# Performance work log

Hardware: AMD Instinct MI355X
Metric: run time of the kernel (lower is better)

## Reference

```python
import jax, jax.numpy as jnp
import numpy as np

B, S, D, M = 8, 32, 256, 2048
TOPK = 8

def setup_inputs() -> dict:
    key = jax.random.key(0)
    ks = jax.random.split(key, 10)
    def lin(kw, fan_in, fan_out):
        # kaiming normal (linear): std = 1/sqrt(fan_in); stored as [in, out]
        return jax.random.normal(kw, (fan_in, fan_out), jnp.float32) / jnp.sqrt(fan_in)
    return {
        "x": jax.random.normal(ks[0], (B, S, D), jnp.float32),
        "memory": jax.random.normal(ks[1], (M, D), jnp.float32) * 0.02,
        "Wq": lin(ks[2], D, D), "bq": jnp.zeros((D,), jnp.float32),
        "Wk": lin(ks[3], D, D), "bk": jnp.zeros((D,), jnp.float32),
        "Wv": lin(ks[4], D, D), "bv": jnp.zeros((D,), jnp.float32),
        "Wg": lin(ks[5], 2 * D, D), "bg": jnp.zeros((D,), jnp.float32),
    }

def reference(x, memory, Wq, bq, Wk, bk, Wv, bv, Wg, bg):
    batch, seq_len, d = x.shape
    scale = jnp.sqrt(jnp.float32(d))
    mem0 = jnp.broadcast_to(memory[None], (batch,) + memory.shape)  # [B,M,D]
    b_idx = jnp.arange(batch)[:, None]

    def step(mem, xt):  # mem [B,M,D], xt [B,D]
        q = xt @ Wq + bq                      # [B,D]
        k = mem @ Wk + bk                     # [B,M,D]
        v = mem @ Wv + bv                     # [B,M,D]
        logits = jnp.einsum('bd,bmd->bm', q, k) / scale
        attn = jax.nn.softmax(logits, axis=-1)            # [B,M]
        out = jnp.einsum('bm,bmd->bd', attn, v)           # [B,D]
        g = jax.nn.sigmoid(jnp.concatenate([xt, out], axis=-1) @ Wg + bg)  # [B,D]
        _, top_idx = jax.lax.top_k(attn, TOPK)            # [B,TOPK]
        old = jnp.take_along_axis(mem, top_idx[:, :, None], axis=1)        # [B,TOPK,D]
        new = (1.0 - g)[:, None, :] * old + g[:, None, :] * xt[:, None, :]
        mem = mem.at[b_idx, top_idx].set(new)
        return mem, out

    _, outs = jax.lax.scan(step, mem0, jnp.swapaxes(x, 0, 1))  # outs [S,B,D]
    return jnp.swapaxes(outs, 0, 1)  # [B,S,D]
```

## Files before the change

### kernel.cpp

```cpp
#include <hip/hip_runtime.h>
#include <math.h>

constexpr int B_ = 8, S_ = 32, D_ = 256, M_ = 2048;
constexpr int N_ = S_ * B_;
constexpr int TK = 8;
constexpr int NSLOT = 256;
constexpr int TOPC = 256;
constexpr int NCAND = NSLOT + TOPC;
constexpr int KSPLIT = 4;
constexpr int CACHE0 = 192;

__global__ __launch_bounds__(256) void k_wvwgT(const float* __restrict__ Wv,
                                               const float* __restrict__ Wg,
                                               const float* __restrict__ bv,
                                               const float* __restrict__ bg,
                                               const float* __restrict__ Wk,
                                               float* __restrict__ WvWgB,
                                               float* __restrict__ bvg,
                                               float* __restrict__ WkT) {
  int blk = blockIdx.x;
  int tid = threadIdx.x;
  if (blk >= 17) {
    __shared__ float tile[32][33];
    int bb = blk - 17;
    int bx = bb & 7, by = bb >> 3;
    int x0 = bx * 32, y0 = by * 32;
    int tx = tid & 31, ty = tid >> 5;
    for (int j = ty; j < 32; j += 8) tile[j][tx] = Wk[(y0 + j) * D_ + x0 + tx];
    __syncthreads();
    for (int j = ty; j < 32; j += 8) WkT[(x0 + j) * D_ + y0 + tx] = tile[tx][j];
    return;
  }
  if (blk == 16) {
    float a = bg[tid];
#pragma unroll 8
    for (int j = 0; j < D_; ++j) a = fmaf(bv[j], Wg[(size_t)(D_ + j) * D_ + tid], a);
    bvg[tid] = a;
    return;
  }
  int i0 = (blk & 3) * 64, d0 = (blk >> 2) * 64;
  __shared__ float At[64 * 64];
  __shared__ float Bt[64 * 64];
  const int r = tid & 63, c = tid >> 6;
  const int lane = tid & 63, wvv = tid >> 6;
  const int tx = lane & 15, ty = lane >> 4;
  const int dg = tx * 4, ig = (wvv * 4 + ty) * 4;
  float acc[4][4];
#pragma unroll
  for (int i = 0; i < 4; ++i)
#pragma unroll
    for (int j = 0; j < 4; ++j) acc[i][j] = 0.f;
  for (int kc = 0; kc < 4; ++kc) {
    __syncthreads();
#pragma unroll
    for (int it = 0; it < 4; ++it) {
      int jq = (c * 4 + it) * 4;
      float4 a = *(const float4*)&Wv[(i0 + r) * D_ + kc * 64 + jq];
      At[(jq + 0) * 64 + r] = a.x; At[(jq + 1) * 64 + r] = a.y;
      At[(jq + 2) * 64 + r] = a.z; At[(jq + 3) * 64 + r] = a.w;
      *(float4*)&Bt[r * 64 + jq] =
          *(const float4*)&Wg[(size_t)(D_ + kc * 64 + r) * D_ + d0 + jq];
    }
    __syncthreads();
#pragma unroll 4
    for (int j = 0; j < 64; ++j) {
      float4 av = *(const float4*)&At[j * 64 + ig];
      float4 bv4 = *(const float4*)&Bt[j * 64 + dg];
      acc[0][0] = fmaf(av.x, bv4.x, acc[0][0]); acc[0][1] = fmaf(av.x, bv4.y, acc[0][1]);
      acc[0][2] = fmaf(av.x, bv4.z, acc[0][2]); acc[0][3] = fmaf(av.x, bv4.w, acc[0][3]);
      acc[1][0] = fmaf(av.y, bv4.x, acc[1][0]); acc[1][1] = fmaf(av.y, bv4.y, acc[1][1]);
      acc[1][2] = fmaf(av.y, bv4.z, acc[1][2]); acc[1][3] = fmaf(av.y, bv4.w, acc[1][3]);
      acc[2][0] = fmaf(av.z, bv4.x, acc[2][0]); acc[2][1] = fmaf(av.z, bv4.y, acc[2][1]);
      acc[2][2] = fmaf(av.z, bv4.z, acc[2][2]); acc[2][3] = fmaf(av.z, bv4.w, acc[2][3]);
      acc[3][0] = fmaf(av.w, bv4.x, acc[3][0]); acc[3][1] = fmaf(av.w, bv4.y, acc[3][1]);
      acc[3][2] = fmaf(av.w, bv4.z, acc[3][2]); acc[3][3] = fmaf(av.w, bv4.w, acc[3][3]);
    }
  }
#pragma unroll
  for (int i = 0; i < 4; ++i)
    *(float4*)&WvWgB[(size_t)(i0 + ig + i) * D_ + d0 + dg] =
        make_float4(acc[i][0], acc[i][1], acc[i][2], acc[i][3]);
}

__global__ __launch_bounds__(256) void k_qproj(
    const float* __restrict__ x, const float* __restrict__ Wq,
    const float* __restrict__ bq, const float* __restrict__ bk,
    const float* __restrict__ WkT, const float* __restrict__ Wg,
    float* __restrict__ qt, float* __restrict__ qbk, float* __restrict__ xgp) {
  int n = blockIdx.x, tid = threadIdx.x;
  int t = n / B_, b = n % B_;
  __shared__ float xr[D_], qsh[D_];
  __shared__ float red[4];
  xr[tid] = x[(b * S_ + t) * D_ + tid];
  __syncthreads();
  float accq = bq[tid], accg = 0.f;
#pragma unroll 8
  for (int i = 0; i < D_; ++i) {
    float xv = xr[i];
    accq = fmaf(xv, Wq[i * D_ + tid], accq);
    accg = fmaf(xv, Wg[i * D_ + tid], accg);
  }
  qsh[tid] = accq;
  xgp[n * D_ + tid] = accg;
  float p = accq * bk[tid];
  for (int off = 32; off > 0; off >>= 1) p += __shfl_down(p, off, 64);
  if ((tid & 63) == 0) red[tid >> 6] = p;
  __syncthreads();
  float acct = 0.f;
#pragma unroll 8
  for (int i = 0; i < D_; ++i) acct = fmaf(qsh[i], WkT[i * D_ + tid], acct);
  qt[n * D_ + tid] = acct;
  if (tid == 0) qbk[n] = red[0] + red[1] + red[2] + red[3];
}

__global__ __launch_bounds__(256) void k_L0(
    const float* __restrict__ qt, const float* __restrict__ mem,
    const float* __restrict__ qbk, float* __restrict__ L0) {
  __shared__ float qtT[64 * 64];
  __shared__ float mT[64 * 64];
  const int tid = threadIdx.x;
  const int m0 = blockIdx.x * 64, n0 = blockIdx.y * 64;
  const int r = tid & 63, c = tid >> 6;
  const int lane = tid & 63, wv = tid >> 6;
  const int tx = lane & 15, ty = lane >> 4;
  const int mg = tx * 4, ng = (wv * 4 + ty) * 4;
  float acc[4][4];
#pragma unroll
  for (int i = 0; i < 4; ++i)
#pragma unroll
    for (int j = 0; j < 4; ++j) acc[i][j] = 0.f;
  for (int kc = 0; kc < 4; ++kc) {
    __syncthreads();
#pragma unroll
    for (int it = 0; it < 4; ++it) {
      int kq = (c * 4 + it) * 4;
      float4 a = *(const float4*)&qt[(n0 + r) * D_ + kc * 64 + kq];
      qtT[(kq + 0) * 64 + r] = a.x; qtT[(kq + 1) * 64 + r] = a.y;
      qtT[(kq + 2) * 64 + r] = a.z; qtT[(kq + 3) * 64 + r] = a.w;
      float4 bm = *(const float4*)&mem[(m0 + r) * D_ + kc * 64 + kq];
      mT[(kq + 0) * 64 + r] = bm.x; mT[(kq + 1) * 64 + r] = bm.y;
      mT[(kq + 2) * 64 + r] = bm.z; mT[(kq + 3) * 64 + r] = bm.w;
    }
    __syncthreads();
#pragma unroll 4
    for (int k = 0; k < 64; ++k) {
      float4 av = *(const float4*)&qtT[k * 64 + ng];
      float4 bv4 = *(const float4*)&mT[k * 64 + mg];
      acc[0][0] = fmaf(av.x, bv4.x, acc[0][0]); acc[0][1] = fmaf(av.x, bv4.y, acc[0][1]);
      acc[0][2] = fmaf(av.x, bv4.z, acc[0][2]); acc[0][3] = fmaf(av.x, bv4.w, acc[0][3]);
      acc[1][0] = fmaf(av.y, bv4.x, acc[1][0]); acc[1][1] = fmaf(av.y, bv4.y, acc[1][1]);
      acc[1][2] = fmaf(av.y, bv4.z, acc[1][2]); acc[1][3] = fmaf(av.y, bv4.w, acc[1][3]);
      acc[2][0] = fmaf(av.z, bv4.x, acc[2][0]); acc[2][1] = fmaf(av.z, bv4.y, acc[2][1]);
      acc[2][2] = fmaf(av.z, bv4.z, acc[2][2]); acc[2][3] = fmaf(av.z, bv4.w, acc[2][3]);
      acc[3][0] = fmaf(av.w, bv4.x, acc[3][0]); acc[3][1] = fmaf(av.w, bv4.y, acc[3][1]);
      acc[3][2] = fmaf(av.w, bv4.z, acc[3][2]); acc[3][3] = fmaf(av.w, bv4.w, acc[3][3]);
    }
  }
#pragma unroll
  for (int i = 0; i < 4; ++i) {
    int n = n0 + ng + i;
    float qbv = qbk[n];
    float4 o;
    o.x = (acc[i][0] + qbv) * 0.0625f; o.y = (acc[i][1] + qbv) * 0.0625f;
    o.z = (acc[i][2] + qbv) * 0.0625f; o.w = (acc[i][3] + qbv) * 0.0625f;
    *(float4*)&L0[n * M_ + m0 + mg] = o;
  }
}

__global__ __launch_bounds__(1024) void k_sortstats(const float* __restrict__ L0,
                                                    float* __restrict__ topv,
                                                    int* __restrict__ topi,
                                                    float* __restrict__ M0,
                                                    double* __restrict__ SumE0) {
  int n = blockIdx.x, tid = threadIdx.x;
  __shared__ float v[M_];
  __shared__ short ix[M_];
  __shared__ double redd[16];
  for (int m = tid; m < M_; m += 1024) {
    v[m] = L0[(size_t)n * M_ + m];
    ix[m] = (short)m;
  }
  __syncthreads();
  for (int size = 2; size <= M_; size <<= 1) {
    for (int stride = size >> 1; stride > 0; stride >>= 1) {
      const int i = tid;
      const int pos = 2 * i - (i & (stride - 1));
      const int j = pos + stride;
      const bool desc = ((pos & size) == 0);
      const float va = v[pos], vb2 = v[j];
      const short ia = ix[pos], ib = ix[j];
      const bool aG = (va > vb2) || (va == vb2 && ia < ib);
      if (desc ? !aG : aG) { v[pos] = vb2; v[j] = va; ix[pos] = ib; ix[j] = ia; }
      __syncthreads();
    }
  }
  if (tid < TOPC) {
    topv[n * TOPC + tid] = v[tid];
    topi[n * TOPC + tid] = (int)ix[tid];
  }
  float mx = v[0];
  if (tid == 0) M0[n] = mx;
  double s = 0.0;
  for (int m = tid; m < M_; m += 1024) s += (double)expf(v[m] - mx);
  for (int off = 32; off > 0; off >>= 1) s += __shfl_down(s, off, 64);
  if ((tid & 63) == 0) redd[tid >> 6] = s;
  __syncthreads();
  if (tid == 0) {
    double t = 0.0;
#pragma unroll
    for (int w = 0; w < 16; ++w) t += redd[w];
    SumE0[n] = t;
  }
}

__global__ __launch_bounds__(256) void k_ctxpart(
    const float* __restrict__ L0, const float* __restrict__ M0,
    const float* __restrict__ mem, float* __restrict__ ctxp) {
  int ks = blockIdx.x;
  int n0 = blockIdx.y * 32;
  int d0 = blockIdx.z * 64;
  int tid = threadIdx.x;
  __shared__ float Et[64 * 32];
  __shared__ float mTl[64 * 64];
  __shared__ float Msh[32];
  if (tid < 32) Msh[tid] = M0[n0 + tid];
  const int lane = tid & 63, wv = tid >> 6;
  const int tx = lane & 15, ty = lane >> 4;
  const int ng = (wv * 4 + ty) * 2;
  const int dg = tx * 4;
  float acc[2][4] = {{0, 0, 0, 0}, {0, 0, 0, 0}};
  for (int kc = 0; kc < 8; ++kc) {
    int kb = ks * 512 + kc * 64;
    __syncthreads();
#pragma unroll
    for (int j = 0; j < 8; ++j) {
      int ii = tid + 256 * j;
      int nr = ii & 31, kk = ii >> 5;
      Et[kk * 32 + nr] = expf(L0[(n0 + nr) * M_ + kb + kk] - Msh[nr]);
    }
    {
      int r = tid & 63, c = tid >> 6;
#pragma unroll
      for (int j = 0; j < 4; ++j) {
        int c4 = (c * 4 + j) * 4;
        *(float4*)&mTl[r * 64 + c4] = *(const float4*)&mem[(kb + r) * D_ + d0 + c4];
      }
    }
    __syncthreads();
#pragma unroll 4
    for (int kk = 0; kk < 64; ++kk) {
      float4 mv = *(const float4*)&mTl[kk * 64 + dg];
      float e0v = Et[kk * 32 + ng], e1v = Et[kk * 32 + ng + 1];
      acc[0][0] = fmaf(e0v, mv.x, acc[0][0]); acc[0][1] = fmaf(e0v, mv.y, acc[0][1]);
      acc[0][2] = fmaf(e0v, mv.z, acc[0][2]); acc[0][3] = fmaf(e0v, mv.w, acc[0][3]);
      acc[1][0] = fmaf(e1v, mv.x, acc[1][0]); acc[1][1] = fmaf(e1v, mv.y, acc[1][1]);
      acc[1][2] = fmaf(e1v, mv.z, acc[1][2]); acc[1][3] = fmaf(e1v, mv.w, acc[1][3]);
    }
  }
#pragma unroll
  for (int i = 0; i < 2; ++i) {
    int n = n0 + ng + i;
    *(float4*)&ctxp[((size_t)ks * N_ + n) * D_ + d0 + dg] =
        make_float4(acc[i][0], acc[i][1], acc[i][2], acc[i][3]);
  }
}

__global__ __launch_bounds__(1024, 4) void k_scan(
    const float* __restrict__ x, const float* __restrict__ mem0,
    const float* __restrict__ Wv, const float* __restrict__ bv,
    const float* __restrict__ WvWgB, const float* __restrict__ bvg,
    const float* __restrict__ qt, const float* __restrict__ qbk,
    const float* __restrict__ xgp, const float* __restrict__ L0,
    const float* __restrict__ M0, const double* __restrict__ SumE0,
    const float* __restrict__ ctxp, const float* __restrict__ topv,
    const int* __restrict__ topi, float* __restrict__ memcur,
    float* __restrict__ out) {
  const int b = blockIdx.x;
  const int tid = threadIdx.x;
  const int lane = tid & 63;
  const int wvid = tid >> 6;

  __shared__ short tpos[M_];
  __shared__ unsigned int descL[NSLOT];
  __shared__ float candV[NCAND];
  __shared__ int candI[NCAND];
  __shared__ float curE[NSLOT], e0sA[NSLOT], diffA[NSLOT];
  __shared__ float dpart[15][D_];
  __shared__ float fpart[15][D_];
  __shared__ float fpart2[15][D_];
  __shared__ float qt_s[2][D_], xt_s[2][D_];
  __shared__ float CTX0_s[D_], xgp_s[D_], g_s[D_], bv_s[D_], bvg_s[D_];
  __shared__ float wvlds[(256 - CACHE0) * D_];
  __shared__ float Msc[S_], qbks[S_];
  __shared__ double sum0s[S_];
  __shared__ float inv_esum;
  __shared__ int Tcount;
  __shared__ int selIdx[TK];

  const float4* mem04 = (const float4*)mem0;
  const float4* mcur4c = (const float4*)memcur;
  float4* mcur4 = (float4*)memcur;
  const float4* Wv4 = (const float4*)Wv;
  const float4* Wg4 = (const float4*)WvWgB;
  const float4* qt4 = (const float4*)qt;
  const float4* x4 = (const float4*)x;
  const float4* ctxp4 = (const float4*)ctxp;
  const float4* xgp4 = (const float4*)xgp;
  const float4* wvlds4 = (const float4*)wvlds;

  float4 wreg[18];
  {
    const int kbase = 17 * wvid;
    if (wvid < 15) {
#pragma unroll
      for (int j = 0; j < 17; ++j) wreg[j] = Wv4[(size_t)(kbase + j) * 64 + lane];
      wreg[17] = (wvid == 14) ? Wv4[(size_t)255 * 64 + lane] : wreg[16];
    }
  }

  for (int m = tid; m < M_; m += 1024) tpos[m] = -1;
  for (int s = tid; s < NSLOT; s += 1024) descL[s] = 0;
  for (int i = tid; i < (256 - CACHE0) * 64; i += 1024)
    ((float4*)wvlds)[i] = Wg4[(size_t)CACHE0 * 64 + i];
  if (tid < NCAND) {
    candV[tid] = -INFINITY;
    candI[tid] = 0x7FFFFFFF;
  }
  if (tid < S_) {
    Msc[tid] = M0[tid * B_ + b];
    qbks[tid] = qbk[tid * B_ + b];
    sum0s[tid] = SumE0[tid * B_ + b];
  } else if (tid >= 64 && tid < 64 + D_) {
    int d = tid - 64;
    bv_s[d] = bv[d];
    bvg_s[d] = bvg[d];
  } else if (tid >= 512 && tid < 576) {
    int j = tid - 512;
    ((float4*)qt_s[0])[j] = qt4[(size_t)b * 64 + j];
  } else if (tid >= 576 && tid < 640) {
    int j = tid - 576;
    ((float4*)xt_s[0])[j] = x4[(size_t)(b * S_) * 64 + j];
  }
  if (tid == 0) Tcount = 0;
  __syncthreads();

  for (int t = 0; t < S_; ++t) {
    const int n = t * B_ + b;
    const int par = t & 1;
    const int Tc = Tcount;
    const float c0 = Msc[t];
    const float qb = qbks[t];

    if (wvid < 15) {
      const float4 qv = ((const float4*)qt_s[par])[lane];
      const float4 g4 = ((const float4*)g_s)[lane];
      const float4 xpv = ((const float4*)xt_s[par ^ 1])[lane];
      float4 acc = make_float4(0.f, 0.f, 0.f, 0.f);
      int s = wvid;
      unsigned int dsc_c = 0;
      float4 mc_c = make_float4(0.f, 0.f, 0.f, 0.f), mo_c = mc_c;
      float l0_c = 0.f;
      if (s < Tc) {
        dsc_c = descL[s];
        const int m = dsc_c & 2047;
        mo_c = mem04[(size_t)m * 64 + lane];
        const bool fromM0 = (dsc_c & (1u << 12)) && (dsc_c & (1u << 11));
        mc_c = fromM0 ? mo_c : mcur4c[(size_t)(b * NSLOT + s) * 64 + lane];
        l0_c = L0[(size_t)n * M_ + m];
      }
      while (s < Tc) {
        const int s2 = s + 15;
        unsigned int dsc_n = 0;
        float4 mc_n = make_float4(0.f, 0.f, 0.f, 0.f), mo_n = mc_n;
        float l0_n = 0.f;
        if (s2 < Tc) {
          dsc_n = descL[s2];
          const int mn = dsc_n & 2047;
          mo_n = mem04[(size_t)mn * 64 + lane];
          const bool fromM0n = (dsc_n & (1u << 12)) && (dsc_n & (1u << 11));
          mc_n = fromM0n ? mo_n : mcur4c[(size_t)(b * NSLOT + s2) * 64 + lane];
          l0_n = L0[(size_t)n * M_ + mn];
        }
        const int m = dsc_c & 2047;
        if (dsc_c & (1u << 12)) {
          mc_c.x = fmaf(g4.x, xpv.x - mc_c.x, mc_c.x);
          mc_c.y = fmaf(g4.y, xpv.y - mc_c.y, mc_c.y);
          mc_c.z = fmaf(g4.z, xpv.z - mc_c.z, mc_c.z);
          mc_c.w = fmaf(g4.w, xpv.w - mc_c.w, mc_c.w);
          mcur4[(size_t)(b * NSLOT + s) * 64 + lane] = mc_c;
          if (lane == 0) descL[s] = (unsigned int)m;
        }
        float p = mc_c.x * qv.x;
        p = fmaf(mc_c.y, qv.y, p);
        p = fmaf(mc_c.z, qv.z, p);
        p = fmaf(mc_c.w, qv.w, p);
#pragma unroll
        for (int off = 1; off < 64; off <<= 1) p += __shfl_xor(p, off, 64);
        const float cur = (p + qb) * 0.0625f;
        const float ce = expf(cur - c0);
        const float e0 = expf(l0_c - c0);
        acc.x = fmaf(ce, mc_c.x, fmaf(-e0, mo_c.x, acc.x));
        acc.y = fmaf(ce, mc_c.y, fmaf(-e0, mo_c.y, acc.y));
        acc.z = fmaf(ce, mc_c.z, fmaf(-e0, mo_c.z, acc.z));
        acc.w = fmaf(ce, mc_c.w, fmaf(-e0, mo_c.w, acc.w));
        if (lane == 0) {
          curE[s] = ce;
          e0sA[s] = e0;
          diffA[s] = ce - e0;
          candV[s] = cur;
          candI[s] = m;
        }
        dsc_c = dsc_n;
        mc_c = mc_n;
        mo_c = mo_n;
        l0_c = l0_n;
        s = s2;
      }
      ((float4*)dpart[wvid])[lane] = acc;
    } else {
#pragma unroll
      for (int jj = 0; jj < 4; ++jj) {
        const int j = lane + jj * 64;
        const int ii = topi[n * TOPC + j];
        const bool fresh = (tpos[ii] < 0);
        candV[NSLOT + j] = fresh ? topv[n * TOPC + j] : -INFINITY;
        candI[NSLOT + j] = fresh ? ii : 0x7FFFFFFF;
      }
      const float4 c0v = ctxp4[(size_t)(0 * N_ + n) * 64 + lane];
      const float4 c1v = ctxp4[(size_t)(1 * N_ + n) * 64 + lane];
      const float4 c2v = ctxp4[(size_t)(2 * N_ + n) * 64 + lane];
      const float4 c3v = ctxp4[(size_t)(3 * N_ + n) * 64 + lane];
      ((float4*)CTX0_s)[lane] = make_float4(c0v.x + c1v.x + c2v.x + c3v.x,
                                            c0v.y + c1v.y + c2v.y + c3v.y,
                                            c0v.z + c1v.z + c2v.z + c3v.z,
                                            c0v.w + c1v.w + c2v.w + c3v.w);
      ((float4*)xgp_s)[lane] = xgp4[(size_t)n * 64 + lane];
      if (t + 1 < S_) {
        ((float4*)qt_s[par ^ 1])[lane] = qt4[(size_t)(n + B_) * 64 + lane];
        ((float4*)xt_s[par ^ 1])[lane] = x4[(size_t)(b * S_ + t + 1) * 64 + lane];
      }
    }
    __syncthreads();

    if (wvid < 15) {
      const int kbase = 17 * wvid;
      const int nr = (wvid == 14) ? 18 : 17;
      float mynum = 0.f;
      if (lane < nr) {
        const int k = (lane == 17) ? 255 : (kbase + lane);
        float nv = CTX0_s[k];
#pragma unroll
        for (int p = 0; p < 15; ++p) nv += dpart[p][k];
        mynum = nv;
      }
      float4 a1 = make_float4(0.f, 0.f, 0.f, 0.f);
      float4 a2 = make_float4(0.f, 0.f, 0.f, 0.f);
#pragma unroll
      for (int j = 0; j < 17; ++j) {
        const float nv = __int_as_float(__builtin_amdgcn_readlane(__float_as_int(mynum), j));
        a1.x = fmaf(nv, wreg[j].x, a1.x); a1.y = fmaf(nv, wreg[j].y, a1.y);
        a1.z = fmaf(nv, wreg[j].z, a1.z); a1.w = fmaf(nv, wreg[j].w, a1.w);
        const int r = kbase + j;
        const float4 w4 = (r >= CACHE0) ? wvlds4[(size_t)(r - CACHE0) * 64 + lane]
                                        : Wg4[(size_t)r * 64 + lane];
        a2.x = fmaf(nv, w4.x, a2.x); a2.y = fmaf(nv, w4.y, a2.y);
        a2.z = fmaf(nv, w4.z, a2.z); a2.w = fmaf(nv, w4.w, a2.w);
      }
      if (wvid == 14) {
        const float nv = __int_as_float(__builtin_amdgcn_readlane(__float_as_int(mynum), 17));
        a1.x = fmaf(nv, wreg[17].x, a1.x); a1.y = fmaf(nv, wreg[17].y, a1.y);
        a1.z = fmaf(nv, wreg[17].z, a1.z); a1.w = fmaf(nv, wreg[17].w, a1.w);
        const float4 w4 = wvlds4[(size_t)(255 - CACHE0) * 64 + lane];
        a2.x = fmaf(nv, w4.x, a2.x); a2.y = fmaf(nv, w4.y, a2.y);
        a2.z = fmaf(nv, w4.z, a2.z); a2.w = fmaf(nv, w4.w, a2.w);
      }
      ((float4*)fpart[wvid])[lane] = a1;
      ((float4*)fpart2[wvid])[lane] = a2;
    } else {
      double ds = 0.0;
      for (int s = lane; s < Tc; s += 64) ds += (double)diffA[s];
      for (int off = 32; off > 0; off >>= 1) ds += __shfl_down(ds, off, 64);
      if (lane == 0) inv_esum = (float)(1.0 / (sum0s[t] + ds));
      if (t + 1 < S_) {
        float cv[8];
        int ci[8];
#pragma unroll
        for (int j = 0; j < 8; ++j) {
          cv[j] = candV[lane * 8 + j];
          ci[j] = candI[lane * 8 + j];
        }
        for (int r = 0; r < TK; ++r) {
          float bvv = cv[0];
          int bii = ci[0];
#pragma unroll
          for (int j = 1; j < 8; ++j)
            if (cv[j] > bvv || (cv[j] == bvv && ci[j] < bii)) { bvv = cv[j]; bii = ci[j]; }
#pragma unroll
          for (int off = 1; off < 64; off <<= 1) {
            float ov = __shfl_xor(bvv, off, 64);
            int oi = __shfl_xor(bii, off, 64);
            if (ov > bvv || (ov == bvv && oi < bii)) { bvv = ov; bii = oi; }
          }
          if (lane == 0) selIdx[r] = bii;
#pragma unroll
          for (int j = 0; j < 8; ++j)
            if (ci[j] == bii) { cv[j] = -INFINITY; ci[j] = 0x7FFFFFFF; }
        }
        if (lane == 0) {
          int tc = Tcount;
          for (int k = 0; k < TK; ++k) {
            const int m = selIdx[k];
            int s = tpos[m];
            unsigned int fresh = 0;
            if (s < 0) {
              s = tc++;
              tpos[m] = (short)s;
              candI[s] = m;
              fresh = 1;
            }
            descL[s] = (unsigned int)m | (fresh << 11) | (1u << 12);
          }
          Tcount = tc;
        }
      }
    }
    __syncthreads();

    if (tid < D_) {
      float o = 0.f;
#pragma unroll
      for (int p = 0; p < 15; ++p) o += fpart[p][tid];
      o = o * inv_esum + bv_s[tid];
      out[((size_t)b * S_ + t) * D_ + tid] = o;
    } else if (tid < 2 * D_) {
      const int d = tid - D_;
      float gg = 0.f;
#pragma unroll
      for (int p = 0; p < 15; ++p) gg += fpart2[p][d];
      const float gin = xgp_s[d] + gg * inv_esum + bvg_s[d];
      g_s[d] = 1.0f / (1.0f + expf(-gin));
    }
    __syncthreads();
  }
}

extern "C" void kernel_launch(void* const* d_in, const int* in_sizes, int n_in,
                              void* d_out, int out_size, void* d_ws, size_t ws_size,
                              hipStream_t stream) {
  const float* x = (const float*)d_in[0];
  const float* mem0 = (const float*)d_in[1];
  const float* Wq = (const float*)d_in[2];
  const float* bq = (const float*)d_in[3];
  const float* Wk = (const float*)d_in[4];
  const float* bk = (const float*)d_in[5];
  const float* Wv = (const float*)d_in[6];
  const float* bv = (const float*)d_in[7];
  const float* Wg = (const float*)d_in[8];
  const float* bg = (const float*)d_in[9];
  float* out = (float*)d_out;
  float* ws = (float*)d_ws;

  size_t o = 0;
  float* WkT = ws + o;    o += (size_t)D_ * D_;
  float* qt = ws + o;     o += (size_t)N_ * D_;
  float* qbk = ws + o;    o += N_;
  float* xgp = ws + o;    o += (size_t)N_ * D_;
  float* L0 = ws + o;     o += (size_t)N_ * M_;
  float* M0 = ws + o;     o += N_;
  double* SumE0 = (double*)(ws + o); o += 2 * N_;
  float* ctxp = ws + o;   o += (size_t)KSPLIT * N_ * D_;
  float* topv = ws + o;   o += (size_t)N_ * TOPC;
  int* topi = (int*)(ws + o); o += (size_t)N_ * TOPC;
  float* WvWgB = ws + o;  o += (size_t)D_ * D_;
  float* bvg = ws + o;    o += D_;
  float* memcur = ws + o; o += (size_t)B_ * NSLOT * D_;

  k_wvwgT<<<dim3(81), dim3(256), 0, stream>>>(Wv, Wg, bv, bg, Wk, WvWgB, bvg, WkT);
  k_qproj<<<dim3(N_), dim3(256), 0, stream>>>(x, Wq, bq, bk, WkT, Wg, qt, qbk, xgp);
  k_L0<<<dim3(M_ / 64, N_ / 64), dim3(256), 0, stream>>>(qt, mem0, qbk, L0);
  k_sortstats<<<dim3(N_), dim3(1024), 0, stream>>>(L0, topv, topi, M0, SumE0);
  k_ctxpart<<<dim3(KSPLIT, N_ / 32, D_ / 64), dim3(256), 0, stream>>>(L0, M0, mem0, ctxp);
  k_scan<<<dim3(B_), dim3(1024), 0, stream>>>(x, mem0, Wv, bv, WvWgB, bvg, qt, qbk, xgp,
                                              L0, M0, SumE0, ctxp, topv, topi, memcur, out);
}
```

Baseline: 612.1 us.

## Batch slot-score reductions and replace serial top-k with bitonic key merge

The per-slot loop in the scan kernel now issues all of a wave's slot loads up front and batches the 64-lane shuffle reductions across up to 17 slots, instead of reducing one slot at a time behind a one-ahead prefetch. The top-8 selection packs each value and index into a 64-bit sortable key, sorts 8 keys per lane with a network, and merges across lanes with butterfly shuffles instead of running eight serial argmax rounds. Slot assignment uses a ballot and popcount across lanes rather than a lane-0 loop, and the esum reduction moves to wave 0. The cost is higher register pressure and a second global reload of the current memory rows.

```diff
diff --git a/kernel.cpp b/kernel.cpp
--- a/kernel.cpp
+++ b/kernel.cpp
@@ -265,6 +265,21 @@
   }
 }
 
+__device__ __forceinline__ unsigned long long shfl_xor_u64(unsigned long long v,
+                                                           int off) {
+  const int lo = __shfl_xor((int)(unsigned)(v & 0xFFFFFFFFull), off, 64);
+  const int hi = __shfl_xor((int)(unsigned)(v >> 32), off, 64);
+  return ((unsigned long long)(unsigned)hi << 32) | (unsigned)lo;
+}
+
+#define CE8(i, jj)                                                  \
+  {                                                                 \
+    const unsigned long long ka_ = key[i], kb_ = key[jj];           \
+    const bool sw_ = kb_ > ka_;                                     \
+    key[i] = sw_ ? kb_ : ka_;                                       \
+    key[jj] = sw_ ? ka_ : kb_;                                      \
+  }
+
 __global__ __launch_bounds__(1024, 4) void k_scan(
     const float* __restrict__ x, const float* __restrict__ mem0,
     const float* __restrict__ Wv, const float* __restrict__ bv,
@@ -282,9 +297,9 @@
 
   __shared__ short tpos[M_];
   __shared__ unsigned int descL[NSLOT];
-  __shared__ float candV[NCAND];
-  __shared__ int candI[NCAND];
-  __shared__ float curE[NSLOT], e0sA[NSLOT], diffA[NSLOT];
+  __shared__ __align__(16) float candV[NCAND];
+  __shared__ __align__(16) int candI[NCAND];
+  __shared__ float e0sA[NSLOT], diffA[NSLOT];
   __shared__ float dpart[15][D_];
   __shared__ float fpart[15][D_];
   __shared__ float fpart2[15][D_];
@@ -295,7 +310,6 @@
   __shared__ double sum0s[S_];
   __shared__ float inv_esum;
   __shared__ int Tcount;
-  __shared__ int selIdx[TK];
 
   const float4* mem04 = (const float4*)mem0;
   const float4* mcur4c = (const float4*)memcur;
@@ -356,65 +370,64 @@
       const float4 g4 = ((const float4*)g_s)[lane];
       const float4 xpv = ((const float4*)xt_s[par ^ 1])[lane];
       float4 acc = make_float4(0.f, 0.f, 0.f, 0.f);
-      int s = wvid;
-      unsigned int dsc_c = 0;
-      float4 mc_c = make_float4(0.f, 0.f, 0.f, 0.f), mo_c = mc_c;
-      float l0_c = 0.f;
-      if (s < Tc) {
-        dsc_c = descL[s];
-        const int m = dsc_c & 2047;
-        mo_c = mem04[(size_t)m * 64 + lane];
-        const bool fromM0 = (dsc_c & (1u << 12)) && (dsc_c & (1u << 11));
-        mc_c = fromM0 ? mo_c : mcur4c[(size_t)(b * NSLOT + s) * 64 + lane];
-        l0_c = L0[(size_t)n * M_ + m];
-      }
-      while (s < Tc) {
-        const int s2 = s + 15;
-        unsigned int dsc_n = 0;
-        float4 mc_n = make_float4(0.f, 0.f, 0.f, 0.f), mo_n = mc_n;
-        float l0_n = 0.f;
-        if (s2 < Tc) {
-          dsc_n = descL[s2];
-          const int mn = dsc_n & 2047;
-          mo_n = mem04[(size_t)mn * 64 + lane];
-          const bool fromM0n = (dsc_n & (1u << 12)) && (dsc_n & (1u << 11));
-          mc_n = fromM0n ? mo_n : mcur4c[(size_t)(b * NSLOT + s2) * 64 + lane];
-          l0_n = L0[(size_t)n * M_ + mn];
+      const int nown = (Tc > wvid) ? ((Tc - wvid + 14) / 15) : 0;
+      float pacc[17];
+#pragma unroll
+      for (int j = 0; j < 17; ++j) {
+        if (j < nown) {
+          const int s = wvid + 15 * j;
+          const unsigned int dsc = descL[s];
+          const int m = dsc & 2047;
+          const float l0v = L0[(size_t)n * M_ + m];
+          const float4 mo = mem04[(size_t)m * 64 + lane];
+          float4 mc;
+          if (dsc & (1u << 12)) {
+            mc = (dsc & (1u << 11)) ? mo
+                                    : mcur4c[(size_t)(b * NSLOT + s) * 64 + lane];
+            mc.x = fmaf(g4.x, xpv.x - mc.x, mc.x);
+            mc.y = fmaf(g4.y, xpv.y - mc.y, mc.y);
+            mc.z = fmaf(g4.z, xpv.z - mc.z, mc.z);
+            mc.w = fmaf(g4.w, xpv.w - mc.w, mc.w);
+            mcur4[(size_t)(b * NSLOT + s) * 64 + lane] = mc;
+            if (lane == 0) descL[s] = (unsigned int)m;
+          } else {
+            mc = mcur4c[(size_t)(b * NSLOT + s) * 64 + lane];
+          }
+          const float e0 = expf(l0v - c0);
+          acc.x = fmaf(-e0, mo.x, acc.x);
+          acc.y = fmaf(-e0, mo.y, acc.y);
+          acc.z = fmaf(-e0, mo.z, acc.z);
+          acc.w = fmaf(-e0, mo.w, acc.w);
+          if (lane == 0) e0sA[s] = e0;
+          float p = mc.x * qv.x;
+          p = fmaf(mc.y, qv.y, p);
+          p = fmaf(mc.z, qv.z, p);
+          p = fmaf(mc.w, qv.w, p);
+          pacc[j] = p;
         }
-        const int m = dsc_c & 2047;
-        if (dsc_c & (1u << 12)) {
-          mc_c.x = fmaf(g4.x, xpv.x - mc_c.x, mc_c.x);
-          mc_c.y = fmaf(g4.y, xpv.y - mc_c.y, mc_c.y);
-          mc_c.z = fmaf(g4.z, xpv.z - mc_c.z, mc_c.z);
-          mc_c.w = fmaf(g4.w, xpv.w - mc_c.w, mc_c.w);
-          mcur4[(size_t)(b * NSLOT + s) * 64 + lane] = mc_c;
-          if (lane == 0) descL[s] = (unsigned int)m;
+      }
+#pragma unroll
+      for (int off = 1; off < 64; off <<= 1) {
+#pragma unroll
+        for (int j = 0; j < 17; ++j)
+          if (j < nown) pacc[j] += __shfl_xor(pacc[j], off, 64);
+      }
+#pragma unroll
+      for (int j = 0; j < 17; ++j) {
+        if (j < nown) {
+          const int s = wvid + 15 * j;
+          const float4 mc = mcur4c[(size_t)(b * NSLOT + s) * 64 + lane];
+          const float cur = (pacc[j] + qb) * 0.0625f;
+          const float ce = expf(cur - c0);
+          acc.x = fmaf(ce, mc.x, acc.x);
+          acc.y = fmaf(ce, mc.y, acc.y);
+          acc.z = fmaf(ce, mc.z, acc.z);
+          acc.w = fmaf(ce, mc.w, acc.w);
+          if (lane == 0) {
+            candV[s] = cur;
+            diffA[s] = ce - e0sA[s];
+          }
         }
-        float p = mc_c.x * qv.x;
-        p = fmaf(mc_c.y, qv.y, p);
-        p = fmaf(mc_c.z, qv.z, p);
-        p = fmaf(mc_c.w, qv.w, p);
-#pragma unroll
-        for (int off = 1; off < 64; off <<= 1) p += __shfl_xor(p, off, 64);
-        const float cur = (p + qb) * 0.0625f;
-        const float ce = expf(cur - c0);
-        const float e0 = expf(l0_c - c0);
-        acc.x = fmaf(ce, mc_c.x, fmaf(-e0, mo_c.x, acc.x));
-        acc.y = fmaf(ce, mc_c.y, fmaf(-e0, mo_c.y, acc.y));
-        acc.z = fmaf(ce, mc_c.z, fmaf(-e0, mo_c.z, acc.z));
-        acc.w = fmaf(ce, mc_c.w, fmaf(-e0, mo_c.w, acc.w));
-        if (lane == 0) {
-          curE[s] = ce;
-          e0sA[s] = e0;
-          diffA[s] = ce - e0;
-          candV[s] = cur;
-          candI[s] = m;
-        }
-        dsc_c = dsc_n;
-        mc_c = mc_n;
-        mo_c = mo_n;
-        l0_c = l0_n;
-        s = s2;
       }
       ((float4*)dpart[wvid])[lane] = acc;
     } else {
@@ -476,53 +489,70 @@
       }
       ((float4*)fpart[wvid])[lane] = a1;
       ((float4*)fpart2[wvid])[lane] = a2;
-    } else {
-      double ds = 0.0;
-      for (int s = lane; s < Tc; s += 64) ds += (double)diffA[s];
-      for (int off = 32; off > 0; off >>= 1) ds += __shfl_down(ds, off, 64);
-      if (lane == 0) inv_esum = (float)(1.0 / (sum0s[t] + ds));
-      if (t + 1 < S_) {
-        float cv[8];
-        int ci[8];
+      if (wvid == 0) {
+        double dsum = 0.0;
+        for (int s2 = lane; s2 < Tc; s2 += 64) dsum += (double)diffA[s2];
+#pragma unroll
+        for (int off = 32; off > 0; off >>= 1) dsum += __shfl_down(dsum, off, 64);
+        if (lane == 0) inv_esum = (float)(1.0 / (sum0s[t] + dsum));
+      }
+    } else if (t + 1 < S_) {
+      const float4 cv0 = ((const float4*)candV)[lane * 2];
+      const float4 cv1 = ((const float4*)candV)[lane * 2 + 1];
+      const int4 ci0 = ((const int4*)candI)[lane * 2];
+      const int4 ci1 = ((const int4*)candI)[lane * 2 + 1];
+      unsigned long long key[8];
+      {
+        const float vs[8] = {cv0.x, cv0.y, cv0.z, cv0.w, cv1.x, cv1.y, cv1.z, cv1.w};
+        const int is[8] = {ci0.x, ci0.y, ci0.z, ci0.w, ci1.x, ci1.y, ci1.z, ci1.w};
 #pragma unroll
         for (int j = 0; j < 8; ++j) {
-          cv[j] = candV[lane * 8 + j];
-          ci[j] = candI[lane * 8 + j];
+          unsigned int bits = __float_as_uint(vs[j]);
+          bits = (bits & 0x80000000u) ? ~bits : (bits | 0x80000000u);
+          key[j] = ((unsigned long long)bits << 11) |
+                   (unsigned long long)(2047 - (is[j] & 2047));
         }
-        for (int r = 0; r < TK; ++r) {
-          float bvv = cv[0];
-          int bii = ci[0];
-#pragma unroll
-          for (int j = 1; j < 8; ++j)
-            if (cv[j] > bvv || (cv[j] == bvv && ci[j] < bii)) { bvv = cv[j]; bii = ci[j]; }
-#pragma unroll
-          for (int off = 1; off < 64; off <<= 1) {
-            float ov = __shfl_xor(bvv, off, 64);
-            int oi = __shfl_xor(bii, off, 64);
-            if (ov > bvv || (ov == bvv && oi < bii)) { bvv = ov; bii = oi; }
-          }
-          if (lane == 0) selIdx[r] = bii;
-#pragma unroll
-          for (int j = 0; j < 8; ++j)
-            if (ci[j] == bii) { cv[j] = -INFINITY; ci[j] = 0x7FFFFFFF; }
+      }
+      CE8(0, 1) CE8(2, 3) CE8(4, 5) CE8(6, 7)
+      CE8(0, 2) CE8(1, 3) CE8(4, 6) CE8(5, 7)
+      CE8(1, 2) CE8(5, 6)
+      CE8(0, 4) CE8(1, 5) CE8(2, 6) CE8(3, 7)
+      CE8(2, 4) CE8(3, 5)
+      CE8(1, 2) CE8(3, 4) CE8(5, 6)
+#pragma unroll
+      for (int off = 1; off < 64; off <<= 1) {
+        unsigned long long pk[8];
+#pragma unroll
+        for (int j = 0; j < 8; ++j) pk[j] = shfl_xor_u64(key[7 - j], off);
+#pragma unroll
+        for (int j = 0; j < 8; ++j) key[j] = (pk[j] > key[j]) ? pk[j] : key[j];
+        CE8(0, 4) CE8(1, 5) CE8(2, 6) CE8(3, 7)
+        CE8(0, 2) CE8(1, 3) CE8(4, 6) CE8(5, 7)
+        CE8(0, 1) CE8(2, 3) CE8(4, 5) CE8(6, 7)
+      }
+      int myM = 2047 - (int)(key[0] & 2047);
+#pragma unroll
+      for (int r = 1; r < TK; ++r) {
+        const int mr = 2047 - (int)(key[r] & 2047);
+        if (lane == r) myM = mr;
+      }
+      int sOld = 0;
+      bool fresh = false;
+      if (lane < TK) {
+        sOld = (int)tpos[myM];
+        fresh = sOld < 0;
+      }
+      const unsigned long long fm = __ballot(fresh);
+      if (lane < TK) {
+        const int before = (int)__popcll(fm & ((1ull << lane) - 1ull));
+        const int snew = fresh ? (Tc + before) : sOld;
+        if (fresh) {
+          tpos[myM] = (short)snew;
+          candI[snew] = myM;
         }
-        if (lane == 0) {
-          int tc = Tcount;
-          for (int k = 0; k < TK; ++k) {
-            const int m = selIdx[k];
-            int s = tpos[m];
-            unsigned int fresh = 0;
-            if (s < 0) {
-              s = tc++;
-              tpos[m] = (short)s;
-              candI[s] = m;
-              fresh = 1;
-            }
-            descL[s] = (unsigned int)m | (fresh << 11) | (1u << 12);
-          }
-          Tcount = tc;
-        }
-      }
+        descL[snew] = (unsigned int)myM | ((fresh ? 1u : 0u) << 11) | (1u << 12);
+      }
+      if (lane == 0) Tcount = Tc + (int)__popcll(fm);
     }
     __syncthreads();
 
```

New measurement: 761.6 us. +24.4%, slower.
